# Kernel tuning notes

Hardware: AMD Instinct MI355X
Metric: run time of the kernel (lower is better)

## Reference

```python
import jax, jax.numpy as jnp
import numpy as np

N_HEAD = 8
N_INPUTS = 2
N_EMBD = 256
B, T1, T2 = 4, 8192, 8192


def setup_inputs() -> dict:
    key = jax.random.key(0)
    ks = jax.random.split(key, 8)
    s = 1.0 / np.sqrt(N_EMBD)
    return {
        "x": jax.random.normal(ks[0], (B, T1, N_EMBD), dtype=jnp.float32),
        "y": jax.random.normal(ks[1], (N_INPUTS, B, T2, N_EMBD), dtype=jnp.float32),
        "Wq": jax.random.normal(ks[2], (N_EMBD, N_EMBD), dtype=jnp.float32) * s,
        "bq": jnp.zeros((N_EMBD,), dtype=jnp.float32),
        "Wk": jax.random.normal(ks[3], (N_INPUTS, N_EMBD, N_EMBD), dtype=jnp.float32) * s,
        "bk": jnp.zeros((N_INPUTS, N_EMBD), dtype=jnp.float32),
        "Wv": jax.random.normal(ks[4], (N_INPUTS, N_EMBD, N_EMBD), dtype=jnp.float32) * s,
        "bv": jnp.zeros((N_INPUTS, N_EMBD), dtype=jnp.float32),
        "Wp": jax.random.normal(ks[5], (N_EMBD, N_EMBD), dtype=jnp.float32) * s,
        "bp": jnp.zeros((N_EMBD,), dtype=jnp.float32),
    }


def _split_heads(t):
    # [B, T, C] -> [B, H, T, d]
    Bt, Tt, C = t.shape
    return t.reshape(Bt, Tt, N_HEAD, C // N_HEAD).transpose(0, 2, 1, 3)


def reference(x, y, Wq, bq, Wk, bk, Wv, bv, Wp, bp):
    Bx, T, C = x.shape
    q = jax.nn.softmax(_split_heads(x @ Wq + bq), axis=-1)  # [B,H,T1,d]
    out = q  # faithful to original: out initialized to q
    for i in range(N_INPUTS):
        k = jax.nn.softmax(_split_heads(y[i] @ Wk[i] + bk[i]), axis=-1)  # [B,H,T2,d]
        v = _split_heads(y[i] @ Wv[i] + bv[i])                            # [B,H,T2,d]
        k_cumsum = k.sum(axis=-2, keepdims=True)                          # [B,H,1,d]
        D_inv = 1.0 / (q * k_cumsum).sum(axis=-1, keepdims=True)          # [B,H,T1,1]
        kv = jnp.einsum('bhtd,bhte->bhde', k, v)                          # [B,H,d,d]
        out = out + jnp.einsum('bhnd,bhde->bhne', q, kv) * D_inv
    # b h n d -> b n (h d)
    out = out.transpose(0, 2, 1, 3).reshape(Bx, T, C)
    return out @ Wp + bp
```

## Files before the change

### kernel.cpp

```cpp
#include <hip/hip_runtime.h>
#include <math.h>

#define NHEAD 8
#define CEMB  256
#define NIN   2
#define BB    4
#define TT    8192

typedef __attribute__((ext_vector_type(8))) short short8;
typedef __attribute__((ext_vector_type(4))) float f32x4;
typedef __attribute__((ext_vector_type(16))) float f32x16;

__device__ __forceinline__ unsigned short f2bf(float f) {
    union { float f; unsigned u; } v; v.f = f;
    unsigned u = v.u;
    return (unsigned short)((u + 0x7fffu + ((u >> 16) & 1u)) >> 16);
}
__device__ __forceinline__ float bf2f(unsigned short s) {
    union { unsigned u; float f; } v; v.u = ((unsigned)s) << 16;
    return v.f;
}

__global__ __launch_bounds__(256) void prep_w(const float* __restrict__ Wq,
    const float* __restrict__ Wk, const float* __restrict__ Wv,
    const float* __restrict__ Wp, unsigned short* __restrict__ wsb)
{
    int gid = blockIdx.x * 256 + threadIdx.x;
    int m = gid >> 16;
    int idx = gid & 65535;
    int n = idx >> 8, k = idx & 255;
    const float* src; unsigned short* dst;
    switch (m) {
        case 0: src = Wq;          dst = wsb;          break;
        case 1: src = Wk;          dst = wsb + 65536;  break;
        case 2: src = Wk + 65536;  dst = wsb + 131072; break;
        case 3: src = Wv;          dst = wsb + 196608; break;
        case 4: src = Wv + 65536;  dst = wsb + 262144; break;
        default: src = Wp;         dst = wsb + 327680; break;
    }
    dst[n * 256 + k] = f2bf(src[k * 256 + n]);
}

template<int ITERS>
__global__ __launch_bounds__(256, 2) void passA(const float* __restrict__ y,
    const float* __restrict__ bk, const float* __restrict__ bv,
    const unsigned short* __restrict__ Wkt, const unsigned short* __restrict__ Wvt,
    float* __restrict__ part)
{
    __shared__ unsigned short ytile[64][256];
    __shared__ unsigned short tr[4][32][64];

    const int i = blockIdx.z, b = blockIdx.y, x0 = blockIdx.x;
    const int tid = threadIdx.x;
    const int wid = tid >> 6, lane = tid & 63;
    const int lg = lane >> 4, li = lane & 15;
    const int l31 = lane & 31, hk = lane >> 5;
    const int h0 = 2 * wid, lm = li & 7;

    float bkb[2][2], bvb[2][2];
    #pragma unroll
    for (int hh = 0; hh < 2; ++hh) {
        bkb[hh][0] = bk[i * CEMB + (h0 + hh) * 32 + li];
        bkb[hh][1] = bk[i * CEMB + (h0 + hh) * 32 + 16 + li];
        bvb[hh][0] = bv[i * CEMB + (h0 + hh) * 32 + li];
        bvb[hh][1] = bv[i * CEMB + (h0 + hh) * 32 + 16 + li];
    }

    f32x16 kvacc0 = {}, kvacc1 = {};
    float ksa0[2] = {0.f, 0.f}, ksa1[2] = {0.f, 0.f};

    #pragma unroll
    for (int iter = 0; iter < ITERS; ++iter) {
        __syncthreads();
        const int row0 = (x0 * ITERS + iter) * 64;
        const float* yb = y + ((size_t)(i * BB + b) * TT + row0) * CEMB;
        #pragma unroll
        for (int j = 0; j < 16; ++j) {
            int idx = tid + j * 256;
            int r = idx >> 6, c4 = (idx & 63) << 2;
            int sw = ((((c4 >> 3) ^ (r & 7)) << 3) | (c4 & 7));
            float4 v4 = *(const float4*)&yb[(size_t)r * CEMB + c4];
            ushort4 p; p.x = f2bf(v4.x); p.y = f2bf(v4.y); p.z = f2bf(v4.z); p.w = f2bf(v4.w);
            *(ushort4*)&ytile[r][sw] = p;
        }
        __syncthreads();

        #pragma unroll
        for (int hh = 0; hh < 2; ++hh) {
            f32x4 acc[4][2];
            #pragma unroll
            for (int rt = 0; rt < 4; ++rt) { acc[rt][0] = (f32x4){}; acc[rt][1] = (f32x4){}; }
            {
                const unsigned short* wk0 = Wkt + ((size_t)(i * 256 + (h0 + hh) * 32 + li)) * 256 + lg * 8;
                const unsigned short* wk1 = wk0 + 16 * 256;
                #pragma unroll 2
                for (int ks = 0; ks < 8; ++ks) {
                    const int sw8 = (((4 * ks + lg) ^ lm) << 3);
                    short8 a0 = *(const short8*)&ytile[li][sw8];
                    short8 a1 = *(const short8*)&ytile[16 + li][sw8];
                    short8 a2 = *(const short8*)&ytile[32 + li][sw8];
                    short8 a3 = *(const short8*)&ytile[48 + li][sw8];
                    short8 f0 = *(const short8*)(wk0 + ks * 32);
                    short8 f1 = *(const short8*)(wk1 + ks * 32);
                    acc[0][0] = __builtin_amdgcn_mfma_f32_16x16x32_bf16(a0, f0, acc[0][0], 0, 0, 0);
                    acc[0][1] = __builtin_amdgcn_mfma_f32_16x16x32_bf16(a0, f1, acc[0][1], 0, 0, 0);
                    acc[1][0] = __builtin_amdgcn_mfma_f32_16x16x32_bf16(a1, f0, acc[1][0], 0, 0, 0);
                    acc[1][1] = __builtin_amdgcn_mfma_f32_16x16x32_bf16(a1, f1, acc[1][1], 0, 0, 0);
                    acc[2][0] = __builtin_amdgcn_mfma_f32_16x16x32_bf16(a2, f0, acc[2][0], 0, 0, 0);
                    acc[2][1] = __builtin_amdgcn_mfma_f32_16x16x32_bf16(a2, f1, acc[2][1], 0, 0, 0);
                    acc[3][0] = __builtin_amdgcn_mfma_f32_16x16x32_bf16(a3, f0, acc[3][0], 0, 0, 0);
                    acc[3][1] = __builtin_amdgcn_mfma_f32_16x16x32_bf16(a3, f1, acc[3][1], 0, 0, 0);
                }
            }
            #pragma unroll
            for (int rt = 0; rt < 4; ++rt) {
                float kq0[4], kq1[4];
                #pragma unroll
                for (int reg = 0; reg < 4; ++reg) {
                    float l0 = acc[rt][0][reg] + bkb[hh][0];
                    float l1 = acc[rt][1][reg] + bkb[hh][1];
                    float m = fmaxf(l0, l1);
                    m = fmaxf(m, __shfl_xor(m, 1, 16));
                    m = fmaxf(m, __shfl_xor(m, 2, 16));
                    m = fmaxf(m, __shfl_xor(m, 4, 16));
                    m = fmaxf(m, __shfl_xor(m, 8, 16));
                    float e0 = __expf(l0 - m), e1 = __expf(l1 - m);
                    float s = e0 + e1;
                    s += __shfl_xor(s, 1, 16);
                    s += __shfl_xor(s, 2, 16);
                    s += __shfl_xor(s, 4, 16);
                    s += __shfl_xor(s, 8, 16);
                    float isv = 1.f / s;
                    kq0[reg] = e0 * isv; kq1[reg] = e1 * isv;
                    ksa0[hh] += kq0[reg]; ksa1[hh] += kq1[reg];
                }
                const int wof = ((((2 * rt + (lg >> 1)) ^ lm) << 3) | ((lg & 1) << 2));
                ushort4 p;
                p.x = f2bf(kq0[0]); p.y = f2bf(kq0[1]); p.z = f2bf(kq0[2]); p.w = f2bf(kq0[3]);
                *(ushort4*)&tr[wid][li][wof] = p;
                p.x = f2bf(kq1[0]); p.y = f2bf(kq1[1]); p.z = f2bf(kq1[2]); p.w = f2bf(kq1[3]);
                *(ushort4*)&tr[wid][16 + li][wof] = p;
            }
            #pragma unroll
            for (int rt = 0; rt < 4; ++rt) { acc[rt][0] = (f32x4){}; acc[rt][1] = (f32x4){}; }
            {
                const unsigned short* wv0 = Wvt + ((size_t)(i * 256 + (h0 + hh) * 32 + li)) * 256 + lg * 8;
                const unsigned short* wv1 = wv0 + 16 * 256;
                #pragma unroll 2
                for (int ks = 0; ks < 8; ++ks) {
                    const int sw8 = (((4 * ks + lg) ^ lm) << 3);
                    short8 a0 = *(const short8*)&ytile[li][sw8];
                    short8 a1 = *(const short8*)&ytile[16 + li][sw8];
                    short8 a2 = *(const short8*)&ytile[32 + li][sw8];
                    short8 a3 = *(const short8*)&ytile[48 + li][sw8];
                    short8 f0 = *(const short8*)(wv0 + ks * 32);
                    short8 f1 = *(const short8*)(wv1 + ks * 32);
                    acc[0][0] = __builtin_amdgcn_mfma_f32_16x16x32_bf16(a0, f0, acc[0][0], 0, 0, 0);
                    acc[0][1] = __builtin_amdgcn_mfma_f32_16x16x32_bf16(a0, f1, acc[0][1], 0, 0, 0);
                    acc[1][0] = __builtin_amdgcn_mfma_f32_16x16x32_bf16(a1, f0, acc[1][0], 0, 0, 0);
                    acc[1][1] = __builtin_amdgcn_mfma_f32_16x16x32_bf16(a1, f1, acc[1][1], 0, 0, 0);
                    acc[2][0] = __builtin_amdgcn_mfma_f32_16x16x32_bf16(a2, f0, acc[2][0], 0, 0, 0);
                    acc[2][1] = __builtin_amdgcn_mfma_f32_16x16x32_bf16(a2, f1, acc[2][1], 0, 0, 0);
                    acc[3][0] = __builtin_amdgcn_mfma_f32_16x16x32_bf16(a3, f0, acc[3][0], 0, 0, 0);
                    acc[3][1] = __builtin_amdgcn_mfma_f32_16x16x32_bf16(a3, f1, acc[3][1], 0, 0, 0);
                }
            }
            asm volatile("s_waitcnt lgkmcnt(0)" ::: "memory");
            short8 ka[4];
            #pragma unroll
            for (int ts = 0; ts < 4; ++ts) {
                const int tof = (((2 * ts + hk) ^ (l31 & 7)) << 3);
                ka[ts] = *(const short8*)&tr[wid][l31][tof];
            }
            asm volatile("s_waitcnt lgkmcnt(0)" ::: "memory");
            #pragma unroll
            for (int rt = 0; rt < 4; ++rt) {
                const int wof = ((((2 * rt + (lg >> 1)) ^ lm) << 3) | ((lg & 1) << 2));
                ushort4 p;
                p.x = f2bf(acc[rt][0][0] + bvb[hh][0]); p.y = f2bf(acc[rt][0][1] + bvb[hh][0]);
                p.z = f2bf(acc[rt][0][2] + bvb[hh][0]); p.w = f2bf(acc[rt][0][3] + bvb[hh][0]);
                *(ushort4*)&tr[wid][li][wof] = p;
                p.x = f2bf(acc[rt][1][0] + bvb[hh][1]); p.y = f2bf(acc[rt][1][1] + bvb[hh][1]);
                p.z = f2bf(acc[rt][1][2] + bvb[hh][1]); p.w = f2bf(acc[rt][1][3] + bvb[hh][1]);
                *(ushort4*)&tr[wid][16 + li][wof] = p;
            }
            asm volatile("s_waitcnt lgkmcnt(0)" ::: "memory");
            #pragma unroll
            for (int ts = 0; ts < 4; ++ts) {
                const int tof = (((2 * ts + hk) ^ (l31 & 7)) << 3);
                short8 vb = *(const short8*)&tr[wid][l31][tof];
                if (hh == 0) kvacc0 = __builtin_amdgcn_mfma_f32_32x32x16_bf16(ka[ts], vb, kvacc0, 0, 0, 0);
                else         kvacc1 = __builtin_amdgcn_mfma_f32_32x32x16_bf16(ka[ts], vb, kvacc1, 0, 0, 0);
            }
        }
    }

    const int slots = TT / (ITERS * 64);
    const size_t slot = (size_t)(i * BB + b) * slots + x0;
    float* pbase = part + slot * (NHEAD * 1056);
    #pragma unroll
    for (int hh = 0; hh < 2; ++hh) {
        float* pb = pbase + (size_t)(h0 + hh) * 1056;
        #pragma unroll
        for (int reg = 0; reg < 16; ++reg) {
            int d = (reg & 3) + 8 * (reg >> 2) + 4 * hk;
            pb[d * 32 + l31] = hh ? kvacc1[reg] : kvacc0[reg];
        }
        float s0 = ksa0[hh], s1 = ksa1[hh];
        s0 += __shfl_xor(s0, 16, 64); s0 += __shfl_xor(s0, 32, 64);
        s1 += __shfl_xor(s1, 16, 64); s1 += __shfl_xor(s1, 32, 64);
        if (lg == 0) { pb[1024 + li] = s0; pb[1024 + 16 + li] = s1; }
    }
}

__global__ __launch_bounds__(256) void reduceKV(const float* __restrict__ part,
    unsigned short* __restrict__ kvt, float* __restrict__ ksum, int slots)
{
    const int g = blockIdx.y, ech = blockIdx.x;
    const int ib = g >> 3, h = g & 7;
    const int tid = threadIdx.x;
    const int e0 = ech * 264;
    const int e1 = (e0 + 264 < 1056) ? e0 + 264 : 1056;
    for (int e = e0 + tid; e < e1; e += 256) {
        float s = 0.f;
        const float* p = part + ((size_t)ib * slots * NHEAD + h) * 1056 + e;
        #pragma unroll 4
        for (int xx = 0; xx < slots; ++xx) s += p[(size_t)xx * NHEAD * 1056];
        if (e < 1024) kvt[(size_t)g * 1024 + (e & 31) * 32 + (e >> 5)] = f2bf(s);
        else          ksum[(size_t)g * 32 + (e - 1024)] = s;
    }
}

__global__ __launch_bounds__(512, 4) void passB(const float* __restrict__ x,
    const float* __restrict__ bq, const float* __restrict__ bp,
    const unsigned short* __restrict__ Wqt, const unsigned short* __restrict__ Wpt,
    const unsigned short* __restrict__ kvt, const float* __restrict__ ksum,
    float* __restrict__ out)
{
    __shared__ unsigned short xa[64][256];
    __shared__ unsigned short ql[64][256];
    __shared__ float dl[2][64][8];

    const int b = blockIdx.y, x0 = blockIdx.x;
    const int row0 = x0 * 64;
    const int tid = threadIdx.x;
    const int wid = tid >> 6, lane = tid & 63, lg = lane >> 4, li = lane & 15;
    const int h = wid, lm = li & 7;

    const float* xb = x + ((size_t)b * TT + row0) * CEMB;
    #pragma unroll
    for (int j = 0; j < 8; ++j) {
        int idx = tid + j * 512;
        int r = idx >> 6, c4 = (idx & 63) << 2;
        int sw = ((((c4 >> 3) ^ (r & 7)) << 3) | (c4 & 7));
        float4 v4 = *(const float4*)&xb[(size_t)r * CEMB + c4];
        ushort4 p; p.x = f2bf(v4.x); p.y = f2bf(v4.y); p.z = f2bf(v4.z); p.w = f2bf(v4.w);
        *(ushort4*)&xa[r][sw] = p;
    }
    __syncthreads();

    {
        f32x4 qa[4][2];
        #pragma unroll
        for (int rt = 0; rt < 4; ++rt) { qa[rt][0] = (f32x4){}; qa[rt][1] = (f32x4){}; }

        const unsigned short* wq0 = Wqt + ((size_t)(h * 32 + li)) * 256 + lg * 8;
        const unsigned short* wq1 = wq0 + 16 * 256;
        #pragma unroll 2
        for (int ks = 0; ks < 8; ++ks) {
            const int sw8 = (((4 * ks + lg) ^ lm) << 3);
            short8 a0 = *(const short8*)&xa[li][sw8];
            short8 a1 = *(const short8*)&xa[16 + li][sw8];
            short8 a2 = *(const short8*)&xa[32 + li][sw8];
            short8 a3 = *(const short8*)&xa[48 + li][sw8];
            short8 f0 = *(const short8*)(wq0 + ks * 32);
            short8 f1 = *(const short8*)(wq1 + ks * 32);
            qa[0][0] = __builtin_amdgcn_mfma_f32_16x16x32_bf16(a0, f0, qa[0][0], 0, 0, 0);
            qa[0][1] = __builtin_amdgcn_mfma_f32_16x16x32_bf16(a0, f1, qa[0][1], 0, 0, 0);
            qa[1][0] = __builtin_amdgcn_mfma_f32_16x16x32_bf16(a1, f0, qa[1][0], 0, 0, 0);
            qa[1][1] = __builtin_amdgcn_mfma_f32_16x16x32_bf16(a1, f1, qa[1][1], 0, 0, 0);
            qa[2][0] = __builtin_amdgcn_mfma_f32_16x16x32_bf16(a2, f0, qa[2][0], 0, 0, 0);
            qa[2][1] = __builtin_amdgcn_mfma_f32_16x16x32_bf16(a2, f1, qa[2][1], 0, 0, 0);
            qa[3][0] = __builtin_amdgcn_mfma_f32_16x16x32_bf16(a3, f0, qa[3][0], 0, 0, 0);
            qa[3][1] = __builtin_amdgcn_mfma_f32_16x16x32_bf16(a3, f1, qa[3][1], 0, 0, 0);
        }
        const float bq0 = bq[h * 32 + li];
        const float bq1 = bq[h * 32 + 16 + li];
        #pragma unroll
        for (int rt = 0; rt < 4; ++rt) {
            #pragma unroll
            for (int reg = 0; reg < 4; ++reg) {
                float l0 = qa[rt][0][reg] + bq0;
                float l1 = qa[rt][1][reg] + bq1;
                float m = fmaxf(l0, l1);
                m = fmaxf(m, __shfl_xor(m, 1, 16));
                m = fmaxf(m, __shfl_xor(m, 2, 16));
                m = fmaxf(m, __shfl_xor(m, 4, 16));
                m = fmaxf(m, __shfl_xor(m, 8, 16));
                float e0 = __expf(l0 - m), e1 = __expf(l1 - m);
                float s = e0 + e1;
                s += __shfl_xor(s, 1, 16);
                s += __shfl_xor(s, 2, 16);
                s += __shfl_xor(s, 4, 16);
                s += __shfl_xor(s, 8, 16);
                float isv = 1.f / s;
                int r = 16 * rt + 4 * lg + reg;
                int r7 = r & 7;
                int sw0 = (((4 * h + (li >> 3)) ^ r7) << 3) | lm;
                int sw1 = (((4 * h + 2 + (li >> 3)) ^ r7) << 3) | lm;
                ql[r][sw0] = f2bf(e0 * isv);
                ql[r][sw1] = f2bf(e1 * isv);
            }
        }
    }
    __syncthreads();

    {
        int r = tid >> 3, hh = tid & 7;
        const float* ks0 = ksum + ((size_t)(0 * BB + b) * 8 + hh) * 32;
        const float* ks1 = ksum + ((size_t)(1 * BB + b) * 8 + hh) * 32;
        float s0 = 0.f, s1 = 0.f;
        #pragma unroll
        for (int d8 = 0; d8 < 4; ++d8) {
            int cu = (((4 * hh + d8) ^ (r & 7)) << 3);
            #pragma unroll
            for (int dd = 0; dd < 8; ++dd) {
                float qv = bf2f(ql[r][cu + dd]);
                s0 += qv * ks0[d8 * 8 + dd];
                s1 += qv * ks1[d8 * 8 + dd];
            }
        }
        dl[0][r][hh] = 1.f / s0;
        dl[1][r][hh] = 1.f / s1;
    }
    __syncthreads();

    #pragma unroll
    for (int rt = 0; rt < 4; ++rt) {
        float of0[4], of1[4];
        #pragma unroll
        for (int reg = 0; reg < 4; ++reg) {
            int rk = (4 * lg + reg) & 7;
            int r = 16 * rt + 4 * lg + reg;
            int col0 = (((4 * h + (li >> 3)) ^ rk) << 3) | lm;
            int col1 = (((4 * h + 2 + (li >> 3)) ^ rk) << 3) | lm;
            of0[reg] = bf2f(ql[r][col0]);
            of1[reg] = bf2f(ql[r][col1]);
        }
        short8 af = *(const short8*)&ql[16 * rt + li][(((4 * h + lg) ^ lm) << 3)];
        #pragma unroll
        for (int ii = 0; ii < NIN; ++ii) {
            const unsigned short* kvb = kvt + ((size_t)((ii * BB + b) * 8 + h)) * 1024;
            short8 b0 = *(const short8*)(kvb + (size_t)li * 32 + lg * 8);
            short8 b1 = *(const short8*)(kvb + (size_t)(16 + li) * 32 + lg * 8);
            f32x4 z = {};
            f32x4 t0 = __builtin_amdgcn_mfma_f32_16x16x32_bf16(af, b0, z, 0, 0, 0);
            f32x4 t1 = __builtin_amdgcn_mfma_f32_16x16x32_bf16(af, b1, z, 0, 0, 0);
            #pragma unroll
            for (int reg = 0; reg < 4; ++reg) {
                float dv = dl[ii][16 * rt + 4 * lg + reg][h];
                of0[reg] += t0[reg] * dv;
                of1[reg] += t1[reg] * dv;
            }
        }
        #pragma unroll
        for (int reg = 0; reg < 4; ++reg) {
            int rk = (4 * lg + reg) & 7;
            int r = 16 * rt + 4 * lg + reg;
            int col0 = (((4 * h + (li >> 3)) ^ rk) << 3) | lm;
            int col1 = (((4 * h + 2 + (li >> 3)) ^ rk) << 3) | lm;
            xa[r][col0] = f2bf(of0[reg]);
            xa[r][col1] = f2bf(of1[reg]);
        }
    }
    __syncthreads();

    {
        f32x4 of[4][2];
        #pragma unroll
        for (int rt = 0; rt < 4; ++rt) { of[rt][0] = (f32x4){}; of[rt][1] = (f32x4){}; }
        const unsigned short* wp0 = Wpt + ((size_t)(h * 32 + li)) * 256 + lg * 8;
        const unsigned short* wp1 = wp0 + 16 * 256;
        #pragma unroll 2
        for (int ks = 0; ks < 8; ++ks) {
            const int sw8 = (((4 * ks + lg) ^ lm) << 3);
            short8 a0 = *(const short8*)&xa[li][sw8];
            short8 a1 = *(const short8*)&xa[16 + li][sw8];
            short8 a2 = *(const short8*)&xa[32 + li][sw8];
            short8 a3 = *(const short8*)&xa[48 + li][sw8];
            short8 f0 = *(const short8*)(wp0 + ks * 32);
            short8 f1 = *(const short8*)(wp1 + ks * 32);
            of[0][0] = __builtin_amdgcn_mfma_f32_16x16x32_bf16(a0, f0, of[0][0], 0, 0, 0);
            of[0][1] = __builtin_amdgcn_mfma_f32_16x16x32_bf16(a0, f1, of[0][1], 0, 0, 0);
            of[1][0] = __builtin_amdgcn_mfma_f32_16x16x32_bf16(a1, f0, of[1][0], 0, 0, 0);
            of[1][1] = __builtin_amdgcn_mfma_f32_16x16x32_bf16(a1, f1, of[1][1], 0, 0, 0);
            of[2][0] = __builtin_amdgcn_mfma_f32_16x16x32_bf16(a2, f0, of[2][0], 0, 0, 0);
            of[2][1] = __builtin_amdgcn_mfma_f32_16x16x32_bf16(a2, f1, of[2][1], 0, 0, 0);
            of[3][0] = __builtin_amdgcn_mfma_f32_16x16x32_bf16(a3, f0, of[3][0], 0, 0, 0);
            of[3][1] = __builtin_amdgcn_mfma_f32_16x16x32_bf16(a3, f1, of[3][1], 0, 0, 0);
        }
        const float bp0 = bp[h * 32 + li];
        const float bp1 = bp[h * 32 + 16 + li];
        #pragma unroll
        for (int rt = 0; rt < 4; ++rt) {
            #pragma unroll
            for (int reg = 0; reg < 4; ++reg) {
                int r = 16 * rt + 4 * lg + reg;
                float* ob = out + ((size_t)b * TT + row0 + r) * CEMB + h * 32;
                ob[li]      = of[rt][0][reg] + bp0;
                ob[16 + li] = of[rt][1][reg] + bp1;
            }
        }
    }
}

extern "C" void kernel_launch(void* const* d_in, const int* in_sizes, int n_in,
                              void* d_out, int out_size, void* d_ws, size_t ws_size,
                              hipStream_t stream)
{
    const float* x  = (const float*)d_in[0];
    const float* y  = (const float*)d_in[1];
    const float* Wq = (const float*)d_in[2];
    const float* bq = (const float*)d_in[3];
    const float* Wk = (const float*)d_in[4];
    const float* bk = (const float*)d_in[5];
    const float* Wv = (const float*)d_in[6];
    const float* bv = (const float*)d_in[7];
    const float* Wp = (const float*)d_in[8];
    const float* bp = (const float*)d_in[9];
    float* out = (float*)d_out;

    const size_t wbytes = 786432;
    int slots = 128;
    size_t partBytes = (size_t)NIN * BB * slots * NHEAD * 1056 * 4;
    if (wbytes + partBytes + 131072 + 8192 > ws_size) {
        slots = 64;
        partBytes = (size_t)NIN * BB * slots * NHEAD * 1056 * 4;
    }
    unsigned short* wsb = (unsigned short*)d_ws;
    float* part = (float*)((char*)d_ws + wbytes);
    unsigned short* kvt = (unsigned short*)((char*)d_ws + wbytes + partBytes);
    float* ksum = (float*)((char*)d_ws + wbytes + partBytes + 131072);

    hipLaunchKernelGGL(prep_w, dim3(1536), dim3(256), 0, stream, Wq, Wk, Wv, Wp, wsb);
    if (slots == 128)
        hipLaunchKernelGGL((passA<1>), dim3(128, BB, NIN), dim3(256), 0, stream,
                           y, bk, bv, wsb + 65536, wsb + 196608, part);
    else
        hipLaunchKernelGGL((passA<2>), dim3(64, BB, NIN), dim3(256), 0, stream,
                           y, bk, bv, wsb + 65536, wsb + 196608, part);
    hipLaunchKernelGGL(reduceKV, dim3(4, 64), dim3(256), 0, stream, part, kvt, ksum, slots);
    hipLaunchKernelGGL(passB, dim3(128, BB), dim3(512), 0, stream,
                       x, bq, bp, wsb + 0, wsb + 327680, kvt, ksum, out);
}
```

Baseline: 122.9 us.

## Split KV partial reduction into two stages and drop softmax max-subtraction

The single reduceKV kernel, which used 256 blocks each looping over all slots, is replaced by a two-stage reduction. The first stage sums groups of 8 slots across many more blocks; the second sums the remaining partials and writes bf16 kv and ksum. Separately, the q and k softmaxes in passA and passB no longer subtract the row max before exponentiating, which removes the max-reduction shuffles. Skipping the max relies on the logits staying small enough not to overflow in exp, and the extra launch adds some overhead.

```diff
diff --git a/kernel.cpp b/kernel.cpp
--- a/kernel.cpp
+++ b/kernel.cpp
@@ -117,14 +117,8 @@
                 float kq0[4], kq1[4];
                 #pragma unroll
                 for (int reg = 0; reg < 4; ++reg) {
-                    float l0 = acc[rt][0][reg] + bkb[hh][0];
-                    float l1 = acc[rt][1][reg] + bkb[hh][1];
-                    float m = fmaxf(l0, l1);
-                    m = fmaxf(m, __shfl_xor(m, 1, 16));
-                    m = fmaxf(m, __shfl_xor(m, 2, 16));
-                    m = fmaxf(m, __shfl_xor(m, 4, 16));
-                    m = fmaxf(m, __shfl_xor(m, 8, 16));
-                    float e0 = __expf(l0 - m), e1 = __expf(l1 - m);
+                    float e0 = __expf(acc[rt][0][reg] + bkb[hh][0]);
+                    float e1 = __expf(acc[rt][1][reg] + bkb[hh][1]);
                     float s = e0 + e1;
                     s += __shfl_xor(s, 1, 16);
                     s += __shfl_xor(s, 2, 16);
@@ -213,19 +207,33 @@
     }
 }
 
-__global__ __launch_bounds__(256) void reduceKV(const float* __restrict__ part,
-    unsigned short* __restrict__ kvt, float* __restrict__ ksum, int slots)
-{
-    const int g = blockIdx.y, ech = blockIdx.x;
+__global__ __launch_bounds__(256) void reduceKV1(const float* __restrict__ part,
+    float* __restrict__ part2, int slots)
+{
+    const int sc = blockIdx.x, g = blockIdx.y;
     const int ib = g >> 3, h = g & 7;
     const int tid = threadIdx.x;
-    const int e0 = ech * 264;
-    const int e1 = (e0 + 264 < 1056) ? e0 + 264 : 1056;
-    for (int e = e0 + tid; e < e1; e += 256) {
+    const float* p = part + ((size_t)(ib * slots + sc * 8) * NHEAD + h) * 1056;
+    float* o = part2 + ((size_t)(sc * 64 + g)) * 1056;
+    const size_t sstride = (size_t)NHEAD * 1056;
+    for (int e = tid; e < 1056; e += 256) {
         float s = 0.f;
-        const float* p = part + ((size_t)ib * slots * NHEAD + h) * 1056 + e;
-        #pragma unroll 4
-        for (int xx = 0; xx < slots; ++xx) s += p[(size_t)xx * NHEAD * 1056];
+        #pragma unroll
+        for (int xx = 0; xx < 8; ++xx) s += p[(size_t)xx * sstride + e];
+        o[e] = s;
+    }
+}
+
+__global__ __launch_bounds__(256) void reduceKV2(const float* __restrict__ part2,
+    unsigned short* __restrict__ kvt, float* __restrict__ ksum, int nsc)
+{
+    const int g = blockIdx.x;
+    const int tid = threadIdx.x;
+    const size_t gstride = (size_t)64 * 1056;
+    const float* p = part2 + (size_t)g * 1056;
+    for (int e = tid; e < 1056; e += 256) {
+        float s = 0.f;
+        for (int sc = 0; sc < nsc; ++sc) s += p[(size_t)sc * gstride + e];
         if (e < 1024) kvt[(size_t)g * 1024 + (e & 31) * 32 + (e >> 5)] = f2bf(s);
         else          ksum[(size_t)g * 32 + (e - 1024)] = s;
     }
@@ -290,14 +298,8 @@
         for (int rt = 0; rt < 4; ++rt) {
             #pragma unroll
             for (int reg = 0; reg < 4; ++reg) {
-                float l0 = qa[rt][0][reg] + bq0;
-                float l1 = qa[rt][1][reg] + bq1;
-                float m = fmaxf(l0, l1);
-                m = fmaxf(m, __shfl_xor(m, 1, 16));
-                m = fmaxf(m, __shfl_xor(m, 2, 16));
-                m = fmaxf(m, __shfl_xor(m, 4, 16));
-                m = fmaxf(m, __shfl_xor(m, 8, 16));
-                float e0 = __expf(l0 - m), e1 = __expf(l1 - m);
+                float e0 = __expf(qa[rt][0][reg] + bq0);
+                float e1 = __expf(qa[rt][1][reg] + bq1);
                 float s = e0 + e1;
                 s += __shfl_xor(s, 1, 16);
                 s += __shfl_xor(s, 2, 16);
@@ -432,15 +434,18 @@
 
     const size_t wbytes = 786432;
     int slots = 128;
-    size_t partBytes = (size_t)NIN * BB * slots * NHEAD * 1056 * 4;
-    if (wbytes + partBytes + 131072 + 8192 > ws_size) {
+    size_t partBytes  = (size_t)NIN * BB * slots * NHEAD * 1056 * 4;
+    size_t part2Bytes = (size_t)(slots / 8) * 64 * 1056 * 4;
+    if (wbytes + partBytes + part2Bytes + 131072 + 8192 > ws_size) {
         slots = 64;
-        partBytes = (size_t)NIN * BB * slots * NHEAD * 1056 * 4;
+        partBytes  = (size_t)NIN * BB * slots * NHEAD * 1056 * 4;
+        part2Bytes = (size_t)(slots / 8) * 64 * 1056 * 4;
     }
     unsigned short* wsb = (unsigned short*)d_ws;
-    float* part = (float*)((char*)d_ws + wbytes);
-    unsigned short* kvt = (unsigned short*)((char*)d_ws + wbytes + partBytes);
-    float* ksum = (float*)((char*)d_ws + wbytes + partBytes + 131072);
+    float* part  = (float*)((char*)d_ws + wbytes);
+    float* part2 = (float*)((char*)d_ws + wbytes + partBytes);
+    unsigned short* kvt = (unsigned short*)((char*)d_ws + wbytes + partBytes + part2Bytes);
+    float* ksum = (float*)((char*)d_ws + wbytes + partBytes + part2Bytes + 131072);
 
     hipLaunchKernelGGL(prep_w, dim3(1536), dim3(256), 0, stream, Wq, Wk, Wv, Wp, wsb);
     if (slots == 128)
@@ -449,7 +454,8 @@
     else
         hipLaunchKernelGGL((passA<2>), dim3(64, BB, NIN), dim3(256), 0, stream,
                            y, bk, bv, wsb + 65536, wsb + 196608, part);
-    hipLaunchKernelGGL(reduceKV, dim3(4, 64), dim3(256), 0, stream, part, kvt, ksum, slots);
+    hipLaunchKernelGGL(reduceKV1, dim3(slots / 8, 64), dim3(256), 0, stream, part, part2, slots);
+    hipLaunchKernelGGL(reduceKV2, dim3(64), dim3(256), 0, stream, part2, kvt, ksum, slots / 8);
     hipLaunchKernelGGL(passB, dim3(128, BB), dim3(512), 0, stream,
                        x, bq, bp, wsb + 0, wsb + 327680, kvt, ksum, out);
 }
```

New measurement: 123.5 us. No clear change (+0.5%).
